# Optimization experiments

Measured on AMD Instinct MI355X. Metric: run time of the kernel, lower is better.

Reference implementation:

```python
import jax, jax.numpy as jnp
import numpy as np

VOCAB_SIZE = 50257


def setup_inputs() -> dict:
    key = jax.random.key(0)
    B, S = 512, 2048
    assignments = jax.random.randint(key, (B, S), 0, VOCAB_SIZE, dtype=jnp.int64)
    # ones_w are the unit weights scattered into the histogram; counting ones == counting occurrences.
    ones_w = jnp.ones((B, S), dtype=jnp.float32)
    return {"assignments": assignments, "ones_w": ones_w}


def reference(assignments, ones_w):
    # Per-row vocab histogram via scatter-add (avoids the O(B*S*V) broadcast-compare
    # intermediate of the original torch code; same math).
    B, S = assignments.shape
    rows = jnp.arange(B)[:, None]                          # (B, 1) broadcast against (B, S)
    counts = jnp.zeros((B, VOCAB_SIZE), dtype=ones_w.dtype).at[rows, assignments].add(ones_w)
    # Normalize each row's histogram to a frequency distribution.
    frequency = counts / jnp.sum(counts, axis=-1, keepdims=True)
    return frequency
```

## Files before the change

kernel.cpp:

```cpp
#include <hip/hip_runtime.h>

#define VOCAB 50257
#define NCHUNK 4
#define CHUNK ((VOCAB + NCHUNK - 1) / NCHUNK)

#define LDS_BARRIER()                                            \
    do {                                                         \
        asm volatile("s_waitcnt lgkmcnt(0)" ::: "memory");       \
        __builtin_amdgcn_s_barrier();                            \
        __builtin_amdgcn_sched_barrier(0);                       \
    } while (0)

__global__ __launch_bounds__(1024) void XTermFrequency_5471788335935_kernel(
    const int* __restrict__ asg, const float* __restrict__ w,
    float* __restrict__ out, int S)
{
    __shared__ float hist[CHUNK];
    __shared__ float s_sum;
    __shared__ float s_inv;

    const int b   = blockIdx.x;
    const int tid = threadIdx.x;
    const long long rowoff = (long long)b * S;
    const int*   __restrict__ row  = asg + rowoff;
    const float* __restrict__ wrow = w   + rowoff;
    float*       __restrict__ orow = out + (long long)b * VOCAB;

    const bool cached = ((S & 1) == 0) && ((S >> 1) == (int)blockDim.x);
    int2   ra = make_int2(0, 0);
    float2 rw = make_float2(0.f, 0.f);
    float  ws = 0.f;
    if (cached) {
        ra = reinterpret_cast<const int2*>(row)[tid];
        rw = reinterpret_cast<const float2*>(wrow)[tid];
        ws = rw.x + rw.y;
    } else {
        for (int s = tid; s < S; s += blockDim.x) ws += wrow[s];
    }

    if (tid == 0) s_sum = 0.f;
    __syncthreads();
    #pragma unroll
    for (int off = 32; off > 0; off >>= 1) ws += __shfl_down(ws, off, 64);
    if ((tid & 63) == 0) atomicAdd(&s_sum, ws);
    __syncthreads();
    if (tid == 0) s_inv = 1.0f / s_sum;

    for (int i = tid; i < CHUNK; i += blockDim.x) hist[i] = 0.f;
    LDS_BARRIER();

    const float inv = s_inv;

    const int phase = b & (NCHUNK - 1);

    for (int cc = 0; cc < NCHUNK; ++cc) {
        const int c  = (cc + phase) & (NCHUNK - 1);
        const int lo = c * CHUNK;

        if (cached) {
            const int v0 = ra.x - lo;
            const int v1 = ra.y - lo;
            if ((unsigned)v0 < (unsigned)CHUNK) atomicAdd(&hist[v0], rw.x);
            if ((unsigned)v1 < (unsigned)CHUNK) atomicAdd(&hist[v1], rw.y);
        } else {
            for (int s = tid; s < S; s += blockDim.x) {
                const int v = row[s] - lo;
                if ((unsigned)v < (unsigned)CHUNK) atomicAdd(&hist[v], wrow[s]);
            }
        }
        LDS_BARRIER();

        const int hi = min(CHUNK, VOCAB - lo);
        for (int i = tid; i < hi; i += blockDim.x) {
            const float h = hist[i];
            hist[i] = 0.f;
            orow[lo + i] = h * inv;
        }
        LDS_BARRIER();
    }
}

extern "C" void kernel_launch(void* const* d_in, const int* in_sizes, int n_in,
                              void* d_out, int out_size, void* d_ws, size_t ws_size,
                              hipStream_t stream) {
    const int*   asg = (const int*)d_in[0];
    const float* w   = (const float*)d_in[1];
    float*       out = (float*)d_out;

    const int B = out_size / VOCAB;
    const int S = in_sizes[0] / B;

    XTermFrequency_5471788335935_kernel<<<B, 1024, 0, stream>>>(asg, w, out, S);
}
```

Before: 23.77 us.

## Use packed 16-bit integer LDS histogram when all weights are one

Adds a runtime check, using a wave ballot, of whether every weight in the row is exactly 1.0. If so, each row is counted with integer atomic adds into a histogram of two 16-bit counters per 32-bit LDS word, which halves the chunk count from four to two. The intent is fewer chunk passes and barriers, and integer rather than float LDS atomics. The float path stays as a fallback, but 16-bit counters assume a bin never reaches 65536, which holds only because S*2 equals blockDim.

```diff
diff --git a/kernel.cpp b/kernel.cpp
--- a/kernel.cpp
+++ b/kernel.cpp
@@ -1,8 +1,11 @@
 #include <hip/hip_runtime.h>
 
-#define VOCAB 50257
-#define NCHUNK 4
-#define CHUNK ((VOCAB + NCHUNK - 1) / NCHUNK)
+#define VOCAB  50257
+#define CHUNKB 25132
+#define NPACK0 12566
+#define NPACK1 12563
+#define NCHUNKF 4
+#define CHUNKF  12566
 
 #define LDS_BARRIER()                                            \
     do {                                                         \
@@ -15,9 +18,9 @@
     const int* __restrict__ asg, const float* __restrict__ w,
     float* __restrict__ out, int S)
 {
-    __shared__ float hist[CHUNK];
+    __shared__ uint32_t h32[NPACK0];
     __shared__ float s_sum;
-    __shared__ float s_inv;
+    __shared__ int   s_ones;
 
     const int b   = blockIdx.x;
     const int tid = threadIdx.x;
@@ -30,53 +33,79 @@
     int2   ra = make_int2(0, 0);
     float2 rw = make_float2(0.f, 0.f);
     float  ws = 0.f;
+    bool   myones = false;
     if (cached) {
         ra = reinterpret_cast<const int2*>(row)[tid];
         rw = reinterpret_cast<const float2*>(wrow)[tid];
         ws = rw.x + rw.y;
+        myones = (rw.x == 1.0f) && (rw.y == 1.0f);
     } else {
         for (int s = tid; s < S; s += blockDim.x) ws += wrow[s];
     }
 
-    if (tid == 0) s_sum = 0.f;
+    if (tid == 0) { s_sum = 0.f; s_ones = cached ? 1 : 0; }
     __syncthreads();
     #pragma unroll
     for (int off = 32; off > 0; off >>= 1) ws += __shfl_down(ws, off, 64);
-    if ((tid & 63) == 0) atomicAdd(&s_sum, ws);
+    const unsigned long long bal = __ballot(myones);
+    if ((tid & 63) == 0) {
+        atomicAdd(&s_sum, ws);
+        if (bal != ~0ull) atomicAnd(&s_ones, 0);
+    }
     __syncthreads();
-    if (tid == 0) s_inv = 1.0f / s_sum;
 
-    for (int i = tid; i < CHUNK; i += blockDim.x) hist[i] = 0.f;
-    LDS_BARRIER();
+    const float inv = 1.0f / s_sum;
 
-    const float inv = s_inv;
-
-    const int phase = b & (NCHUNK - 1);
-
-    for (int cc = 0; cc < NCHUNK; ++cc) {
-        const int c  = (cc + phase) & (NCHUNK - 1);
-        const int lo = c * CHUNK;
-
-        if (cached) {
-            const int v0 = ra.x - lo;
-            const int v1 = ra.y - lo;
-            if ((unsigned)v0 < (unsigned)CHUNK) atomicAdd(&hist[v0], rw.x);
-            if ((unsigned)v1 < (unsigned)CHUNK) atomicAdd(&hist[v1], rw.y);
-        } else {
-            for (int s = tid; s < S; s += blockDim.x) {
-                const int v = row[s] - lo;
-                if ((unsigned)v < (unsigned)CHUNK) atomicAdd(&hist[v], wrow[s]);
+    if (s_ones) {
+        for (int j = tid; j < NPACK0; j += 1024) h32[j] = 0u;
+        LDS_BARRIER();
+        const int phase = b & 1;
+        #pragma unroll
+        for (int cc = 0; cc < 2; ++cc) {
+            const int c  = cc ^ phase;
+            const int lo = c * CHUNKB;
+            const int np = c ? NPACK1 : NPACK0;
+            const int v0 = ra.x - lo, v1 = ra.y - lo;
+            if ((unsigned)v0 < (unsigned)CHUNKB)
+                atomicAdd(&h32[v0 >> 1], 1u << ((v0 & 1) << 4));
+            if ((unsigned)v1 < (unsigned)CHUNKB)
+                atomicAdd(&h32[v1 >> 1], 1u << ((v1 & 1) << 4));
+            LDS_BARRIER();
+            for (int j = tid; j < np; j += 1024) {
+                const uint32_t wd = h32[j];
+                h32[j] = 0u;
+                const int i0 = lo + (j << 1);
+                orow[i0] = (float)(wd & 0xffffu) * inv;
+                if (i0 + 1 < VOCAB)
+                    orow[i0 + 1] = (float)(wd >> 16) * inv;
             }
+            LDS_BARRIER();
         }
+    } else {
+        float* hf = reinterpret_cast<float*>(h32);
+        for (int i = tid; i < CHUNKF; i += blockDim.x) hf[i] = 0.f;
         LDS_BARRIER();
-
-        const int hi = min(CHUNK, VOCAB - lo);
-        for (int i = tid; i < hi; i += blockDim.x) {
-            const float h = hist[i];
-            hist[i] = 0.f;
-            orow[lo + i] = h * inv;
+        for (int c = 0; c < NCHUNKF; ++c) {
+            const int lo = c * CHUNKF;
+            if (cached) {
+                const int v0 = ra.x - lo, v1 = ra.y - lo;
+                if ((unsigned)v0 < (unsigned)CHUNKF) atomicAdd(&hf[v0], rw.x);
+                if ((unsigned)v1 < (unsigned)CHUNKF) atomicAdd(&hf[v1], rw.y);
+            } else {
+                for (int s = tid; s < S; s += blockDim.x) {
+                    const int v = row[s] - lo;
+                    if ((unsigned)v < (unsigned)CHUNKF) atomicAdd(&hf[v], wrow[s]);
+                }
+            }
+            LDS_BARRIER();
+            const int hi = min(CHUNKF, VOCAB - lo);
+            for (int i = tid; i < hi; i += blockDim.x) {
+                const float h = hf[i];
+                hf[i] = 0.f;
+                orow[lo + i] = h * inv;
+            }
+            LDS_BARRIER();
         }
-        LDS_BARRIER();
     }
 }
 
```

Result: slower. 27.73 us (+16.7%).
